# Optimization experiments

Measured on AMD Instinct MI355X. Metric: run time of the kernel, lower is better.

Reference implementation:

```python
import jax, jax.numpy as jnp
import numpy as np


def gcn_conv(x, edge_index, edge_weight, W, b):
    """PyG-style GCNConv: h = x @ W; add self-loops (w=1); sym deg^-1/2 norm;
    scatter-add aggregation; + bias."""
    N = x.shape[0]
    h = x @ W                                   # [N, F_out]
    row, col = edge_index[0], edge_index[1]     # src, dst
    loop = jnp.arange(N)
    row = jnp.concatenate([row, loop])
    col = jnp.concatenate([col, loop])
    ew = jnp.concatenate([edge_weight, jnp.ones((N,), edge_weight.dtype)])
    deg = jax.ops.segment_sum(ew, col, num_segments=N)
    dinv = jnp.where(deg > 0, deg ** -0.5, 0.0)
    norm = dinv[row] * ew * dinv[col]           # [E+N]
    out = jax.ops.segment_sum(h[row] * norm[:, None], col, num_segments=N)
    return out + b


def setup_inputs() -> dict:
    key = jax.random.key(0)
    ks = jax.random.split(key, 12)
    N, F_in, H, O, E = 20000, 3000, 512, 256, 640000
    x = jax.random.normal(ks[0], (N, F_in), dtype=jnp.float32)
    sim_edge_index = jax.random.randint(ks[1], (2, E), 0, N, dtype=jnp.int64)
    sim_edge_weight = jax.random.uniform(ks[2], (E,), dtype=jnp.float32)
    dist_edge_index = jax.random.randint(ks[3], (2, E), 0, N, dtype=jnp.int64)
    dist_edge_weight = jax.random.uniform(ks[4], (E,), dtype=jnp.float32)
    s = 0.02
    return {
        "x": x,
        "sim_edge_index": sim_edge_index,
        "sim_edge_weight": sim_edge_weight,
        "dist_edge_index": dist_edge_index,
        "dist_edge_weight": dist_edge_weight,
        "W1": jax.random.normal(ks[5], (F_in, H), dtype=jnp.float32) * s,
        "b1": jnp.zeros((H,), jnp.float32),
        "W2": jax.random.normal(ks[6], (F_in, H), dtype=jnp.float32) * s,
        "b2": jnp.zeros((H,), jnp.float32),
        "Ws": jax.random.normal(ks[7], (H, O), dtype=jnp.float32) * s,
        "bs": jnp.zeros((O,), jnp.float32),
        "Wd": jax.random.normal(ks[8], (H, O), dtype=jnp.float32) * s,
        "bd": jnp.zeros((O,), jnp.float32),
        "Wf": jax.random.normal(ks[9], (2 * O, O), dtype=jnp.float32) * s,
        "bf": jnp.zeros((O,), jnp.float32),
    }


def reference(x, sim_edge_index, sim_edge_weight, dist_edge_index,
              dist_edge_weight, W1, b1, W2, b2, Ws, bs, Wd, bd, Wf, bf):
    # eval mode: dropout is identity
    xs = jax.nn.relu(gcn_conv(x, sim_edge_index, sim_edge_weight, W1, b1))
    xd = jax.nn.relu(gcn_conv(x, dist_edge_index, dist_edge_weight, W2, b2))
    x_sim = gcn_conv(xs, sim_edge_index, sim_edge_weight, Ws, bs)
    x_dist = gcn_conv(xd, dist_edge_index, dist_edge_weight, Wd, bd)
    fused = jnp.concatenate([x_sim, x_dist], axis=1) @ Wf + bf
    return (x_sim, x_dist, fused)
```

## Files before the change

### kernel.cpp

```cpp
#include <hip/hip_runtime.h>
#include <cstdint>
#include <cstddef>

typedef unsigned short u16;
typedef __bf16 bf16x8 __attribute__((ext_vector_type(8)));
typedef float f32x4 __attribute__((ext_vector_type(4)));

#define N_NODES 20000
#define MPAD    20096
#define E_EDGES 640000
#define K1      3000
#define K1P     3008
#define H_DIM   512
#define NW      1024
#define O_DIM   256

__device__ __forceinline__ float bf2f(unsigned int hi) {
  union { unsigned int u; float f; } v; v.u = hi << 16; return v.f;
}
__device__ __forceinline__ u16 f2bf(float f) {
  union { float f; unsigned int u; } v; v.f = f;
  unsigned int u = v.u;
  return (u16)((u + 0x7fffu + ((u >> 16) & 1u)) >> 16);
}

__device__ __forceinline__ void gl2lds16(const void* g, void* l) {
  __builtin_amdgcn_global_load_lds((const __attribute__((address_space(1))) void*)g,
                                   (__attribute__((address_space(3))) void*)l, 16, 0, 0);
}

__global__ __launch_bounds__(256) void deg_init_k(float* degS, float* degD, int* cntS, int* cntD) {
  int i = blockIdx.x * 256 + threadIdx.x;
  if (i < N_NODES) { degS[i] = 1.0f; degD[i] = 1.0f; cntS[i] = 0; cntD[i] = 0; }
}

__global__ __launch_bounds__(256) void deg_accum_k(const int* eiS, const float* ewS,
                                                   const int* eiD, const float* ewD,
                                                   float* degS, float* degD, int* cntS, int* cntD) {
  int e = blockIdx.x * 256 + threadIdx.x;
  if (e < E_EDGES) {
    int cs = eiS[E_EDGES + e];
    atomicAdd(&degS[cs], ewS[e]);
    atomicAdd(&cntS[cs], 1);
    int cd = eiD[E_EDGES + e];
    atomicAdd(&degD[cd], ewD[e]);
    atomicAdd(&cntD[cd], 1);
  }
}

__global__ __launch_bounds__(256) void dinv_k(const float* degS, const float* degD,
                                              float* dinvS, float* dinvD) {
  int i = blockIdx.x * 256 + threadIdx.x;
  if (i < N_NODES) { dinvS[i] = rsqrtf(degS[i]); dinvD[i] = rsqrtf(degD[i]); }
}

__global__ __launch_bounds__(1024) void scan_k(const int* cntS, int* offS, int* curS,
                                               const int* cntD, int* offD, int* curD) {
  const int* cnt = blockIdx.x ? cntD : cntS;
  int* off = blockIdx.x ? offD : offS;
  int* cur = blockIdx.x ? curD : curS;
  __shared__ int sums[1024];
  const int t = threadIdx.x;
  const int CH = 20;
  int base = t * CH;
  int s = 0;
  for (int j = 0; j < CH; ++j) { int idx = base + j; if (idx < N_NODES) s += cnt[idx]; }
  sums[t] = s;
  __syncthreads();
  for (int d = 1; d < 1024; d <<= 1) {
    int v = (t >= d) ? sums[t - d] : 0;
    __syncthreads();
    sums[t] += v;
    __syncthreads();
  }
  int run = sums[t] - s;
  for (int j = 0; j < CH; ++j) {
    int idx = base + j;
    if (idx <= N_NODES) {
      off[idx] = run; cur[idx] = run;
      if (idx < N_NODES) run += cnt[idx];
    }
  }
}

__global__ __launch_bounds__(256) void scatter_k(const int* eiS, const float* ewS, const float* dinvS,
                                                 int* curS, int* ssrcS, float* snrmS,
                                                 const int* eiD, const float* ewD, const float* dinvD,
                                                 int* curD, int* ssrcD, float* snrmD) {
  int e = blockIdx.x * 256 + threadIdx.x;
  if (e < E_EDGES) {
    {
      int r = eiS[e], c = eiS[E_EDGES + e];
      int pos = atomicAdd(&curS[c], 1);
      ssrcS[pos] = r;
      snrmS[pos] = dinvS[r] * ewS[e] * dinvS[c];
    }
    {
      int r = eiD[e], c = eiD[E_EDGES + e];
      int pos = atomicAdd(&curD[c], 1);
      ssrcD[pos] = r;
      snrmD[pos] = dinvD[r] * ewD[e] * dinvD[c];
    }
  }
}

__global__ __launch_bounds__(256) void conv_x_k(const float* __restrict__ x, u16* __restrict__ xb) {
  const int row = blockIdx.x;
  for (int c = threadIdx.x; c < 376; c += 256) {
    uint4 o = {0, 0, 0, 0};
    if (row < N_NODES && c < 375) {
      const float4* p = (const float4*)(x + (size_t)row * K1 + (size_t)c * 8);
      float4 v0 = p[0], v1 = p[1];
      o.x = f2bf(v0.x) | ((unsigned)f2bf(v0.y) << 16);
      o.y = f2bf(v0.z) | ((unsigned)f2bf(v0.w) << 16);
      o.z = f2bf(v1.x) | ((unsigned)f2bf(v1.y) << 16);
      o.w = f2bf(v1.z) | ((unsigned)f2bf(v1.w) << 16);
    }
    *(uint4*)(xb + (size_t)row * K1P + (size_t)c * 8) = o;
  }
}

__global__ __launch_bounds__(256) void conv_w12_k(const float* __restrict__ W1,
                                                  const float* __restrict__ W2,
                                                  u16* __restrict__ w12t) {
  __shared__ float t[64][65];
  const int kb = blockIdx.x;
  const int nb = blockIdx.y;
  const int n0 = nb * 64;
  const float* W = (n0 < H_DIM) ? W1 : W2;
  const int nn0 = n0 & (H_DIM - 1);
  const int k0 = kb * 64;
  const int tc = threadIdx.x & 63;
  const int tr4 = threadIdx.x >> 6;
#pragma unroll
  for (int rr = 0; rr < 16; ++rr) {
    int r = tr4 * 16 + rr;
    int k = k0 + r;
    t[r][tc] = (k < K1) ? W[(size_t)k * H_DIM + nn0 + tc] : 0.f;
  }
  __syncthreads();
#pragma unroll
  for (int rr = 0; rr < 16; ++rr) {
    int n = tr4 * 16 + rr;
    w12t[(size_t)(n0 + n) * K1P + k0 + tc] = f2bf(t[tc][n]);
  }
}

__global__ __launch_bounds__(256) void conv_wsm_k(const float* Ws, const float* Wd, const float* Wf,
                                                  u16* wst, u16* wdt, u16* wft) {
  __shared__ float t[64][65];
  const int which = blockIdx.z;
  const float* W = (which == 0) ? Ws : (which == 1) ? Wd : Wf;
  u16* o = (which == 0) ? wst : (which == 1) ? wdt : wft;
  const int k0 = blockIdx.x * 64;
  const int n0 = blockIdx.y * 64;
  const int tc = threadIdx.x & 63;
  const int tr4 = threadIdx.x >> 6;
#pragma unroll
  for (int rr = 0; rr < 16; ++rr) {
    int r = tr4 * 16 + rr;
    t[r][tc] = W[(size_t)(k0 + r) * O_DIM + n0 + tc];
  }
  __syncthreads();
#pragma unroll
  for (int rr = 0; rr < 16; ++rr) {
    int n = tr4 * 16 + rr;
    o[(size_t)(n0 + n) * H_DIM + k0 + tc] = f2bf(t[tc][n]);
  }
}

template <typename CT, bool BIAS>
__global__ __launch_bounds__(256) void gemm_bt(const u16* __restrict__ A, const u16* __restrict__ Bt,
                                               CT* __restrict__ C, const float* __restrict__ bias,
                                               int Mreal, int K, int ldc) {
  __shared__ alignas(16) u16 As[128 * 64];
  __shared__ alignas(16) u16 Bs[128 * 64];
  const int tid = threadIdx.x;
  const int lane = tid & 63;
  const int wv = tid >> 6;
  const int bm = blockIdx.y * 128;
  const int bn = blockIdx.x * 128;

  const int wm = (wv >> 1) << 6;
  const int wn = (wv & 1) << 6;
  const int frow = lane & 15;
  const int q = lane >> 4;
  const int r7 = lane & 7;

  const int srow = tid >> 3;
  const int sgr = ((tid & 7) ^ ((tid >> 3) & 7)) << 3;
  const u16* ga = A + (size_t)(bm + srow) * K + sgr;
  const u16* gb = Bt + (size_t)(bn + srow) * K + sgr;
  u16* la = &As[wv * 512];
  u16* lb = &Bs[wv * 512];

  f32x4 acc[4][4] = {};

  for (int k0 = 0; k0 < K; k0 += 64) {
#pragma unroll
    for (int r = 0; r < 4; ++r) {
      gl2lds16(ga + (size_t)(r * 32) * K + k0, la + r * 2048);
      gl2lds16(gb + (size_t)(r * 32) * K + k0, lb + r * 2048);
    }
    __syncthreads();
#pragma unroll
    for (int ks = 0; ks < 64; ks += 32) {
      const int p = (((q + (ks >> 3)) ^ r7) << 3);
      bf16x8 af[4], bv[4];
#pragma unroll
      for (int t = 0; t < 4; ++t) {
        af[t] = *(const bf16x8*)&As[(wm + t * 16 + frow) * 64 + p];
        bv[t] = *(const bf16x8*)&Bs[(wn + t * 16 + frow) * 64 + p];
      }
#pragma unroll
      for (int i = 0; i < 4; ++i)
#pragma unroll
        for (int j = 0; j < 4; ++j)
          acc[i][j] = __builtin_amdgcn_mfma_f32_16x16x32_bf16(af[i], bv[j], acc[i][j], 0, 0, 0);
    }
    __syncthreads();
  }

  const int crow = (lane >> 4) << 2;
  const int ccol = lane & 15;
#pragma unroll
  for (int i = 0; i < 4; ++i) {
#pragma unroll
    for (int r = 0; r < 4; ++r) {
      int gr = bm + wm + i * 16 + crow + r;
      if (gr < Mreal) {
#pragma unroll
        for (int j = 0; j < 4; ++j) {
          int gc = bn + wn + j * 16 + ccol;
          float v = acc[i][j][r];
          if constexpr (BIAS) v += bias[gc];
          if constexpr (sizeof(CT) == 2) C[(size_t)gr * ldc + gc] = (CT)f2bf(v);
          else C[(size_t)gr * ldc + gc] = (CT)v;
        }
      }
    }
  }
}

__global__ __launch_bounds__(256) void agg1_k(const u16* __restrict__ h12,
                                              const int* offS, const int* srcS, const float* nrmS,
                                              const float* dinvS, const float* b1,
                                              const int* offD, const int* srcD, const float* nrmD,
                                              const float* dinvD, const float* b2,
                                              u16* __restrict__ xsd) {
  const int lane = threadIdx.x & 63;
  const int wv = threadIdx.x >> 6;
  const int i = blockIdx.x * 4 + wv;
  const int g = blockIdx.y;
  if (i >= MPAD) return;
  u16* outp = xsd + ((size_t)g * MPAD + i) * H_DIM + lane * 8;
  if (i >= N_NODES) { uint4 z = {0, 0, 0, 0}; *(uint4*)outp = z; return; }

  const int* off = g ? offD : offS;
  const int* src = g ? srcD : srcS;
  const float* nrm = g ? nrmD : nrmS;
  const float* dinv = g ? dinvD : dinvS;
  const float* bias = g ? b2 : b1;
  const u16* hb = h12 + (size_t)g * H_DIM + lane * 8;

  float a[8];
  float dv = dinv[i];
  float sw = dv * dv;
  uint4 u = *(const uint4*)(hb + (size_t)i * NW);
  a[0] = sw * bf2f(u.x & 0xffff); a[1] = sw * bf2f(u.x >> 16);
  a[2] = sw * bf2f(u.y & 0xffff); a[3] = sw * bf2f(u.y >> 16);
  a[4] = sw * bf2f(u.z & 0xffff); a[5] = sw * bf2f(u.z >> 16);
  a[6] = sw * bf2f(u.w & 0xffff); a[7] = sw * bf2f(u.w >> 16);

  const int e0 = off[i], e1 = off[i + 1];
  int e = e0;
  for (; e + 4 <= e1; e += 4) {
    int ss[4]; float ww[4];
#pragma unroll
    for (int t = 0; t < 4; ++t) { ss[t] = src[e + t]; ww[t] = nrm[e + t]; }
    uint4 vv[4];
#pragma unroll
    for (int t = 0; t < 4; ++t) vv[t] = *(const uint4*)(hb + (size_t)ss[t] * NW);
#pragma unroll
    for (int t = 0; t < 4; ++t) {
      float w = ww[t]; uint4 v = vv[t];
      a[0] += w * bf2f(v.x & 0xffff); a[1] += w * bf2f(v.x >> 16);
      a[2] += w * bf2f(v.y & 0xffff); a[3] += w * bf2f(v.y >> 16);
      a[4] += w * bf2f(v.z & 0xffff); a[5] += w * bf2f(v.z >> 16);
      a[6] += w * bf2f(v.w & 0xffff); a[7] += w * bf2f(v.w >> 16);
    }
  }
  for (; e < e1; ++e) {
    int s = src[e];
    float w = nrm[e];
    uint4 v = *(const uint4*)(hb + (size_t)s * NW);
    a[0] += w * bf2f(v.x & 0xffff); a[1] += w * bf2f(v.x >> 16);
    a[2] += w * bf2f(v.y & 0xffff); a[3] += w * bf2f(v.y >> 16);
    a[4] += w * bf2f(v.z & 0xffff); a[5] += w * bf2f(v.z >> 16);
    a[6] += w * bf2f(v.w & 0xffff); a[7] += w * bf2f(v.w >> 16);
  }
  float4 bA = *(const float4*)(bias + lane * 8);
  float4 bB = *(const float4*)(bias + lane * 8 + 4);
  a[0] = fmaxf(a[0] + bA.x, 0.f); a[1] = fmaxf(a[1] + bA.y, 0.f);
  a[2] = fmaxf(a[2] + bA.z, 0.f); a[3] = fmaxf(a[3] + bA.w, 0.f);
  a[4] = fmaxf(a[4] + bB.x, 0.f); a[5] = fmaxf(a[5] + bB.y, 0.f);
  a[6] = fmaxf(a[6] + bB.z, 0.f); a[7] = fmaxf(a[7] + bB.w, 0.f);
  uint4 o;
  o.x = f2bf(a[0]) | ((unsigned)f2bf(a[1]) << 16);
  o.y = f2bf(a[2]) | ((unsigned)f2bf(a[3]) << 16);
  o.z = f2bf(a[4]) | ((unsigned)f2bf(a[5]) << 16);
  o.w = f2bf(a[6]) | ((unsigned)f2bf(a[7]) << 16);
  *(uint4*)outp = o;
}

__global__ __launch_bounds__(256) void agg2_k(const u16* __restrict__ hsb, const u16* __restrict__ hdb,
                                              const int* offS, const int* srcS, const float* nrmS,
                                              const float* dinvS, const float* bs,
                                              const int* offD, const int* srcD, const float* nrmD,
                                              const float* dinvD, const float* bd,
                                              float* __restrict__ outF, u16* __restrict__ xcat) {
  const int lane = threadIdx.x & 63;
  const int wv = threadIdx.x >> 6;
  const int i = blockIdx.x * 4 + wv;
  const int g = blockIdx.y;
  if (i >= MPAD) return;
  u16* oc = xcat + (size_t)i * H_DIM + (size_t)g * O_DIM + lane * 4;
  if (i >= N_NODES) { uint2 z = {0, 0}; *(uint2*)oc = z; return; }

  const u16* h = g ? hdb : hsb;
  const int* off = g ? offD : offS;
  const int* src = g ? srcD : srcS;
  const float* nrm = g ? nrmD : nrmS;
  const float* dinv = g ? dinvD : dinvS;
  const float* bias = g ? bd : bs;
  const u16* hb = h + lane * 4;

  float a[4];
  float dv = dinv[i];
  float sw = dv * dv;
  uint2 u = *(const uint2*)(hb + (size_t)i * O_DIM);
  a[0] = sw * bf2f(u.x & 0xffff); a[1] = sw * bf2f(u.x >> 16);
  a[2] = sw * bf2f(u.y & 0xffff); a[3] = sw * bf2f(u.y >> 16);

  const int e0 = off[i], e1 = off[i + 1];
  int e = e0;
  for (; e + 8 <= e1; e += 8) {
    int ss[8]; float ww[8];
#pragma unroll
    for (int t = 0; t < 8; ++t) { ss[t] = src[e + t]; ww[t] = nrm[e + t]; }
    uint2 vv[8];
#pragma unroll
    for (int t = 0; t < 8; ++t) vv[t] = *(const uint2*)(hb + (size_t)ss[t] * O_DIM);
#pragma unroll
    for (int t = 0; t < 8; ++t) {
      float w = ww[t]; uint2 v = vv[t];
      a[0] += w * bf2f(v.x & 0xffff); a[1] += w * bf2f(v.x >> 16);
      a[2] += w * bf2f(v.y & 0xffff); a[3] += w * bf2f(v.y >> 16);
    }
  }
  for (; e < e1; ++e) {
    int s = src[e];
    float w = nrm[e];
    uint2 v = *(const uint2*)(hb + (size_t)s * O_DIM);
    a[0] += w * bf2f(v.x & 0xffff); a[1] += w * bf2f(v.x >> 16);
    a[2] += w * bf2f(v.y & 0xffff); a[3] += w * bf2f(v.y >> 16);
  }
  float4 bb = *(const float4*)(bias + lane * 4);
  a[0] += bb.x; a[1] += bb.y; a[2] += bb.z; a[3] += bb.w;

  float4 fo = {a[0], a[1], a[2], a[3]};
  *(float4*)(outF + (size_t)g * N_NODES * O_DIM + (size_t)i * O_DIM + lane * 4) = fo;
  uint2 o;
  o.x = f2bf(a[0]) | ((unsigned)f2bf(a[1]) << 16);
  o.y = f2bf(a[2]) | ((unsigned)f2bf(a[3]) << 16);
  *(uint2*)oc = o;
}

extern "C" void kernel_launch(void* const* d_in, const int* in_sizes, int n_in,
                              void* d_out, int out_size, void* d_ws, size_t ws_size,
                              hipStream_t stream) {
  const float* x = (const float*)d_in[0];
  const int* eiS = (const int*)d_in[1];
  const float* ewS = (const float*)d_in[2];
  const int* eiD = (const int*)d_in[3];
  const float* ewD = (const float*)d_in[4];
  const float* W1 = (const float*)d_in[5];
  const float* b1 = (const float*)d_in[6];
  const float* W2 = (const float*)d_in[7];
  const float* b2 = (const float*)d_in[8];
  const float* Ws = (const float*)d_in[9];
  const float* bs = (const float*)d_in[10];
  const float* Wd = (const float*)d_in[11];
  const float* bd = (const float*)d_in[12];
  const float* Wf = (const float*)d_in[13];
  const float* bf_ = (const float*)d_in[14];
  float* out = (float*)d_out;

  char* p = (char*)d_ws;
  auto alloc = [&](size_t n) -> char* { char* r = p; p += (n + 255) & ~(size_t)255; return r; };

  u16* xb    = (u16*)alloc((size_t)MPAD * K1P * 2);
  u16* w12t  = (u16*)alloc((size_t)NW * K1P * 2);
  u16* h12   = (u16*)alloc((size_t)N_NODES * NW * 2);
  u16* xsd   = (u16*)alloc((size_t)2 * MPAD * H_DIM * 2);
  u16* hsb   = (u16*)alloc((size_t)N_NODES * O_DIM * 2);
  u16* hdb   = (u16*)alloc((size_t)N_NODES * O_DIM * 2);
  u16* xcat  = (u16*)alloc((size_t)MPAD * H_DIM * 2);
  u16* wst   = (u16*)alloc((size_t)O_DIM * H_DIM * 2);
  u16* wdt   = (u16*)alloc((size_t)O_DIM * H_DIM * 2);
  u16* wft   = (u16*)alloc((size_t)O_DIM * H_DIM * 2);
  float* degS = (float*)alloc((size_t)N_NODES * 4);
  float* degD = (float*)alloc((size_t)N_NODES * 4);
  float* dinvS = (float*)alloc((size_t)N_NODES * 4);
  float* dinvD = (float*)alloc((size_t)N_NODES * 4);
  int* cntS = (int*)alloc((size_t)N_NODES * 4);
  int* cntD = (int*)alloc((size_t)N_NODES * 4);
  int* offS = (int*)alloc((size_t)(N_NODES + 1) * 4);
  int* offD = (int*)alloc((size_t)(N_NODES + 1) * 4);
  int* curS = (int*)alloc((size_t)(N_NODES + 1) * 4);
  int* curD = (int*)alloc((size_t)(N_NODES + 1) * 4);
  int* ssrcS = (int*)alloc((size_t)E_EDGES * 4);
  int* ssrcD = (int*)alloc((size_t)E_EDGES * 4);
  float* snrmS = (float*)alloc((size_t)E_EDGES * 4);
  float* snrmD = (float*)alloc((size_t)E_EDGES * 4);

  const int gN = (N_NODES + 255) / 256;
  const int gE = (E_EDGES + 255) / 256;

  deg_init_k<<<gN, 256, 0, stream>>>(degS, degD, cntS, cntD);
  deg_accum_k<<<gE, 256, 0, stream>>>(eiS, ewS, eiD, ewD, degS, degD, cntS, cntD);
  dinv_k<<<gN, 256, 0, stream>>>(degS, degD, dinvS, dinvD);
  scan_k<<<2, 1024, 0, stream>>>(cntS, offS, curS, cntD, offD, curD);
  scatter_k<<<gE, 256, 0, stream>>>(eiS, ewS, dinvS, curS, ssrcS, snrmS,
                                    eiD, ewD, dinvD, curD, ssrcD, snrmD);

  conv_x_k<<<MPAD, 256, 0, stream>>>(x, xb);
  conv_w12_k<<<dim3(47, 16), 256, 0, stream>>>(W1, W2, w12t);
  conv_wsm_k<<<dim3(8, 4, 3), 256, 0, stream>>>(Ws, Wd, Wf, wst, wdt, wft);

  gemm_bt<u16, false><<<dim3(8, 157), 256, 0, stream>>>(xb, w12t, h12, nullptr, N_NODES, K1P, NW);

  agg1_k<<<dim3(MPAD / 4, 2), 256, 0, stream>>>(h12, offS, ssrcS, snrmS, dinvS, b1,
                                                offD, ssrcD, snrmD, dinvD, b2, xsd);

  gemm_bt<u16, false><<<dim3(2, 157), 256, 0, stream>>>(xsd, wst, hsb, nullptr, N_NODES, H_DIM, O_DIM);
  gemm_bt<u16, false><<<dim3(2, 157), 256, 0, stream>>>(xsd + (size_t)MPAD * H_DIM, wdt, hdb, nullptr,
                                                        N_NODES, H_DIM, O_DIM);

  agg2_k<<<dim3(MPAD / 4, 2), 256, 0, stream>>>(hsb, hdb, offS, ssrcS, snrmS, dinvS, bs,
                                                offD, ssrcD, snrmD, dinvD, bd, out, xcat);

  gemm_bt<float, true><<<dim3(2, 157), 256, 0, stream>>>(xcat, wft, out + (size_t)2 * N_NODES * O_DIM,
                                                         bf_, N_NODES, H_DIM, O_DIM);
}
```

Measured before the change: 1.076 ms.

## Fuse fp32-to-bf16 conversion of x into first GEMM and batch small GEMMs

Removes the separate kernel that converts x to a padded bf16 copy. The first GEMM now loads fp32 x directly, converts it to bf16 in registers and writes it to LDS, which avoids writing and re-reading the intermediate buffer. Block indices are remapped so that the eight column tiles sharing a row block run close together, improving L2 reuse of the fp32 rows. The two per-branch second-layer GEMMs are merged into one launch using blockIdx.z. In exchange, the A tile is loaded synchronously through registers rather than asynchronously. The last K chunk also reads up to 8 floats past the end of each row, which is multiplied by zero-padded weights but reads slightly out of bounds on the final row.

New measurement: 1.078 ms. About the same (+0.2%).

```diff
diff --git a/kernel.cpp b/kernel.cpp
--- a/kernel.cpp
+++ b/kernel.cpp
@@ -104,22 +104,6 @@
   }
 }
 
-__global__ __launch_bounds__(256) void conv_x_k(const float* __restrict__ x, u16* __restrict__ xb) {
-  const int row = blockIdx.x;
-  for (int c = threadIdx.x; c < 376; c += 256) {
-    uint4 o = {0, 0, 0, 0};
-    if (row < N_NODES && c < 375) {
-      const float4* p = (const float4*)(x + (size_t)row * K1 + (size_t)c * 8);
-      float4 v0 = p[0], v1 = p[1];
-      o.x = f2bf(v0.x) | ((unsigned)f2bf(v0.y) << 16);
-      o.y = f2bf(v0.z) | ((unsigned)f2bf(v0.w) << 16);
-      o.z = f2bf(v1.x) | ((unsigned)f2bf(v1.y) << 16);
-      o.w = f2bf(v1.z) | ((unsigned)f2bf(v1.w) << 16);
-    }
-    *(uint4*)(xb + (size_t)row * K1P + (size_t)c * 8) = o;
-  }
-}
-
 __global__ __launch_bounds__(256) void conv_w12_k(const float* __restrict__ W1,
                                                   const float* __restrict__ W2,
                                                   u16* __restrict__ w12t) {
@@ -170,9 +154,9 @@
 }
 
 template <typename CT, bool BIAS>
-__global__ __launch_bounds__(256) void gemm_bt(const u16* __restrict__ A, const u16* __restrict__ Bt,
-                                               CT* __restrict__ C, const float* __restrict__ bias,
-                                               int Mreal, int K, int ldc) {
+__device__ __forceinline__ void gemm_body(const u16* __restrict__ A, const u16* __restrict__ Bt,
+                                          CT* __restrict__ C, const float* __restrict__ bias,
+                                          int Mreal, int K, int ldc) {
   __shared__ alignas(16) u16 As[128 * 64];
   __shared__ alignas(16) u16 Bs[128 * 64];
   const int tid = threadIdx.x;
@@ -236,6 +220,104 @@
           if constexpr (BIAS) v += bias[gc];
           if constexpr (sizeof(CT) == 2) C[(size_t)gr * ldc + gc] = (CT)f2bf(v);
           else C[(size_t)gr * ldc + gc] = (CT)v;
+        }
+      }
+    }
+  }
+}
+
+__global__ __launch_bounds__(256) void gemm_pair_k(const u16* A0, const u16* B0, u16* C0,
+                                                   const u16* A1, const u16* B1, u16* C1) {
+  const u16* A = blockIdx.z ? A1 : A0;
+  const u16* Bt = blockIdx.z ? B1 : B0;
+  u16* C = blockIdx.z ? C1 : C0;
+  gemm_body<u16, false>(A, Bt, C, nullptr, N_NODES, H_DIM, O_DIM);
+}
+
+__global__ __launch_bounds__(256) void gemm_f_k(const u16* A, const u16* Bt, float* C,
+                                                const float* bias) {
+  gemm_body<float, true>(A, Bt, C, bias, N_NODES, H_DIM, O_DIM);
+}
+
+__global__ __launch_bounds__(256) void gemm_x_k(const float* __restrict__ X,
+                                                const u16* __restrict__ Bt,
+                                                u16* __restrict__ C) {
+  __shared__ alignas(16) u16 As[128 * 64];
+  __shared__ alignas(16) u16 Bs[128 * 64];
+  const int tid = threadIdx.x;
+  const int lane = tid & 63;
+  const int wv = tid >> 6;
+
+  const int h = blockIdx.y * 8 + blockIdx.x;
+  const int chunk = 157;
+  const int L = (h & 7) * chunk + (h >> 3);
+  const int bn = (L & 7) * 128;
+  const int bm = (L >> 3) * 128;
+
+  const int wm = (wv >> 1) << 6;
+  const int wn = (wv & 1) << 6;
+  const int frow = lane & 15;
+  const int q = lane >> 4;
+  const int r7 = lane & 7;
+
+  const int srow = tid >> 3;
+  const int lgr = (tid & 7) ^ (srow & 7);
+  const float* xa[4];
+#pragma unroll
+  for (int r = 0; r < 4; ++r) {
+    int row = bm + srow + r * 32;
+    if (row >= N_NODES) row = 0;
+    xa[r] = X + (size_t)row * K1 + lgr * 8;
+  }
+  const u16* gb = Bt + (size_t)(bn + srow) * K1P + (lgr << 3);
+  u16* lb = &Bs[wv * 512];
+
+  f32x4 acc[4][4] = {};
+
+  for (int k0 = 0; k0 < K1P; k0 += 64) {
+#pragma unroll
+    for (int r = 0; r < 4; ++r)
+      gl2lds16(gb + (size_t)(r * 32) * K1P + k0, lb + r * 2048);
+#pragma unroll
+    for (int r = 0; r < 4; ++r) {
+      float4 v0 = *(const float4*)(xa[r] + k0);
+      float4 v1 = *(const float4*)(xa[r] + k0 + 4);
+      bf16x8 pk;
+      pk[0] = (__bf16)v0.x; pk[1] = (__bf16)v0.y; pk[2] = (__bf16)v0.z; pk[3] = (__bf16)v0.w;
+      pk[4] = (__bf16)v1.x; pk[5] = (__bf16)v1.y; pk[6] = (__bf16)v1.z; pk[7] = (__bf16)v1.w;
+      *(bf16x8*)&As[r * 2048 + tid * 8] = pk;
+    }
+    __syncthreads();
+#pragma unroll
+    for (int ks = 0; ks < 64; ks += 32) {
+      const int p = (((q + (ks >> 3)) ^ r7) << 3);
+      bf16x8 af[4], bv[4];
+#pragma unroll
+      for (int t = 0; t < 4; ++t) {
+        af[t] = *(const bf16x8*)&As[(wm + t * 16 + frow) * 64 + p];
+        bv[t] = *(const bf16x8*)&Bs[(wn + t * 16 + frow) * 64 + p];
+      }
+#pragma unroll
+      for (int i = 0; i < 4; ++i)
+#pragma unroll
+        for (int j = 0; j < 4; ++j)
+          acc[i][j] = __builtin_amdgcn_mfma_f32_16x16x32_bf16(af[i], bv[j], acc[i][j], 0, 0, 0);
+    }
+    __syncthreads();
+  }
+
+  const int crow = (lane >> 4) << 2;
+  const int ccol = lane & 15;
+#pragma unroll
+  for (int i = 0; i < 4; ++i) {
+#pragma unroll
+    for (int r = 0; r < 4; ++r) {
+      int gr = bm + wm + i * 16 + crow + r;
+      if (gr < N_NODES) {
+#pragma unroll
+        for (int j = 0; j < 4; ++j) {
+          int gc = bn + wn + j * 16 + ccol;
+          C[(size_t)gr * NW + gc] = f2bf(acc[i][j][r]);
         }
       }
     }
@@ -399,7 +481,6 @@
   char* p = (char*)d_ws;
   auto alloc = [&](size_t n) -> char* { char* r = p; p += (n + 255) & ~(size_t)255; return r; };
 
-  u16* xb    = (u16*)alloc((size_t)MPAD * K1P * 2);
   u16* w12t  = (u16*)alloc((size_t)NW * K1P * 2);
   u16* h12   = (u16*)alloc((size_t)N_NODES * NW * 2);
   u16* xsd   = (u16*)alloc((size_t)2 * MPAD * H_DIM * 2);
@@ -434,22 +515,19 @@
   scatter_k<<<gE, 256, 0, stream>>>(eiS, ewS, dinvS, curS, ssrcS, snrmS,
                                     eiD, ewD, dinvD, curD, ssrcD, snrmD);
 
-  conv_x_k<<<MPAD, 256, 0, stream>>>(x, xb);
   conv_w12_k<<<dim3(47, 16), 256, 0, stream>>>(W1, W2, w12t);
   conv_wsm_k<<<dim3(8, 4, 3), 256, 0, stream>>>(Ws, Wd, Wf, wst, wdt, wft);
 
-  gemm_bt<u16, false><<<dim3(8, 157), 256, 0, stream>>>(xb, w12t, h12, nullptr, N_NODES, K1P, NW);
+  gemm_x_k<<<dim3(8, 157), 256, 0, stream>>>(x, w12t, h12);
 
   agg1_k<<<dim3(MPAD / 4, 2), 256, 0, stream>>>(h12, offS, ssrcS, snrmS, dinvS, b1,
                                                 offD, ssrcD, snrmD, dinvD, b2, xsd);
 
-  gemm_bt<u16, false><<<dim3(2, 157), 256, 0, stream>>>(xsd, wst, hsb, nullptr, N_NODES, H_DIM, O_DIM);
-  gemm_bt<u16, false><<<dim3(2, 157), 256, 0, stream>>>(xsd + (size_t)MPAD * H_DIM, wdt, hdb, nullptr,
-                                                        N_NODES, H_DIM, O_DIM);
+  gemm_pair_k<<<dim3(2, 157, 2), 256, 0, stream>>>(xsd, wst, hsb,
+                                                   xsd + (size_t)MPAD * H_DIM, wdt, hdb);
 
   agg2_k<<<dim3(MPAD / 4, 2), 256, 0, stream>>>(hsb, hdb, offS, ssrcS, snrmS, dinvS, bs,
                                                 offD, ssrcD, snrmD, dinvD, bd, out, xcat);
 
-  gemm_bt<float, true><<<dim3(2, 157), 256, 0, stream>>>(xcat, wft, out + (size_t)2 * N_NODES * O_DIM,
-                                                         bf_, N_NODES, H_DIM, O_DIM);
-}
+  gemm_f_k<<<dim3(2, 157), 256, 0, stream>>>(xcat, wft, out + (size_t)2 * N_NODES * O_DIM, bf_);
+}
```
